# Optimization experiments

Measured on AMD Instinct MI355X. Metric: run time of the kernel, lower is better.

## Reference

```python
import jax, jax.numpy as jnp
import numpy as np

NUM_POINTS = 17
T_MAX = 2.0
VAR_GAMMA = 1.0
EPS = 1e-8


def setup_inputs() -> dict:
    key = jax.random.key(0)
    k1, k2 = jax.random.split(key)
    embeddings = jax.random.normal(k1, (65536, 768), dtype=jnp.float32)
    directions = jax.random.normal(k2, (768, 64), dtype=jnp.float32)
    return {"embeddings": embeddings, "directions": directions}


def reference(embeddings, directions):
    z = embeddings.astype(jnp.float32)  # [B, D]

    # per-dim variance floor (torch .std is unbiased, ddof=1)
    cls_std = jnp.std(z, axis=0, ddof=1)
    var_floor = jnp.mean(jax.nn.relu(VAR_GAMMA - cls_std))

    # column-normalized random directions (F.normalize(dim=0))
    dirs = directions / jnp.linalg.norm(directions, axis=0, keepdims=True)
    proj = z @ dirs  # [B, S]
    std = jnp.std(proj, axis=0, ddof=1)
    proj = (proj - jnp.mean(proj, axis=0, keepdims=True)) / (std + EPS)

    # trapezoidal quadrature over t in (0, T_MAX]
    t = jnp.linspace(0.0, T_MAX, NUM_POINTS + 1)[1:]  # [T]
    dt = T_MAX / NUM_POINTS
    w = jnp.full((NUM_POINTS,), dt).at[0].set(dt / 2).at[-1].set(dt / 2)

    # ECF over all t at once: tp [T, B, S]
    tp = t[:, None, None] * proj[None]
    ecf_real = jnp.mean(jnp.cos(tp), axis=1)  # [T, S]
    ecf_imag = jnp.mean(jnp.sin(tp), axis=1)  # [T, S]
    ecf_sq = ecf_real ** 2 + ecf_imag ** 2
    tcf = jnp.exp(-0.5 * t ** 2)[:, None]  # [T, 1]
    per_t = jnp.mean(ecf_sq - 2.0 * ecf_real * tcf + tcf ** 2, axis=1)  # [T]
    total = jnp.sum(w * per_t)

    loss = total + var_floor
    return loss
```

## Files before the change

kernel.cpp:

```cpp
#include <hip/hip_runtime.h>
#include <math.h>

#define B_ROWS 65536
#define D_DIM  768
#define S_DIM  64
#define T_PTS  17

#define WS_COLSUM 0
#define WS_COLSQ  768
#define WS_PSUM   1536
#define WS_PSQ    1600
#define WS_ECFR   1664
#define WS_ECFI   2752
#define WS_INVN   3840
#define WS_PROJ   4096

__global__ void norm_kernel(const float* __restrict__ dirs, float* __restrict__ ws) {
    int s = blockIdx.x;
    int t = threadIdx.x;
    if (s < 60) ws[s * 64 + t] = 0.f;
    float sum = 0.f;
    #pragma unroll
    for (int j = 0; j < D_DIM / 64; ++j) {
        float v = dirs[(size_t)(t + j * 64) * S_DIM + s];
        sum += v * v;
    }
    #pragma unroll
    for (int off = 32; off > 0; off >>= 1)
        sum += __shfl_down(sum, off, 64);
    if (t == 0) ws[WS_INVN + s] = 1.0f / sqrtf(sum);
}

__global__ __launch_bounds__(256) void gemm_kernel(const float* __restrict__ z,
                                                   const float* __restrict__ dirs,
                                                   float* __restrict__ ws) {
    __shared__ float smem[4352 + 4096];
    __shared__ float red_s[16 * 64];
    __shared__ float red_q[16 * 64];
    float* zsT = smem;
    float* dsm = smem + 4352;
    float* proj = ws + WS_PROJ;

    int tid = threadIdx.x;
    int tx = tid & 15, ty = tid >> 4;
    size_t rowbase = (size_t)blockIdx.x * 64;

    float4 invn4 = *reinterpret_cast<const float4*>(ws + WS_INVN + tx * 4);
    float acc[4][4] = {};

    for (int c = 0; c < D_DIM / 64; ++c) {
        int kc = c * 64;
        float ps0 = 0, ps1 = 0, ps2 = 0, ps3 = 0;
        float pq0 = 0, pq1 = 0, pq2 = 0, pq3 = 0;
        #pragma unroll
        for (int j = 0; j < 4; ++j) {
            int rr = ty + 16 * j;
            float4 v = *reinterpret_cast<const float4*>(
                z + (rowbase + rr) * D_DIM + kc + tx * 4);
            zsT[(tx * 4 + 0) * 68 + rr] = v.x;
            zsT[(tx * 4 + 1) * 68 + rr] = v.y;
            zsT[(tx * 4 + 2) * 68 + rr] = v.z;
            zsT[(tx * 4 + 3) * 68 + rr] = v.w;
            ps0 += v.x; pq0 = fmaf(v.x, v.x, pq0);
            ps1 += v.y; pq1 = fmaf(v.y, v.y, pq1);
            ps2 += v.z; pq2 = fmaf(v.z, v.z, pq2);
            ps3 += v.w; pq3 = fmaf(v.w, v.w, pq3);
            float4 dv = *reinterpret_cast<const float4*>(
                dirs + (size_t)(kc + rr) * S_DIM + tx * 4);
            dv.x *= invn4.x; dv.y *= invn4.y; dv.z *= invn4.z; dv.w *= invn4.w;
            *reinterpret_cast<float4*>(dsm + rr * 64 + tx * 4) = dv;
        }
        red_s[ty * 64 + tx * 4 + 0] = ps0;  red_q[ty * 64 + tx * 4 + 0] = pq0;
        red_s[ty * 64 + tx * 4 + 1] = ps1;  red_q[ty * 64 + tx * 4 + 1] = pq1;
        red_s[ty * 64 + tx * 4 + 2] = ps2;  red_q[ty * 64 + tx * 4 + 2] = pq2;
        red_s[ty * 64 + tx * 4 + 3] = ps3;  red_q[ty * 64 + tx * 4 + 3] = pq3;
        __syncthreads();

        if (tid < 64) {
            float ss = 0, qq = 0;
            #pragma unroll
            for (int r = 0; r < 16; ++r) {
                ss += red_s[r * 64 + tid];
                qq += red_q[r * 64 + tid];
            }
            atomicAdd(&ws[WS_COLSUM + kc + tid], ss);
            atomicAdd(&ws[WS_COLSQ + kc + tid], qq);
        }

        #pragma unroll 8
        for (int k = 0; k < 64; ++k) {
            float4 a4 = *reinterpret_cast<const float4*>(zsT + k * 68 + ty * 4);
            float4 b4 = *reinterpret_cast<const float4*>(dsm + k * 64 + tx * 4);
            float av[4] = {a4.x, a4.y, a4.z, a4.w};
            float bv[4] = {b4.x, b4.y, b4.z, b4.w};
            #pragma unroll
            for (int i = 0; i < 4; ++i)
                #pragma unroll
                for (int j = 0; j < 4; ++j)
                    acc[i][j] = fmaf(av[i], bv[j], acc[i][j]);
        }
        __syncthreads();
    }

    #pragma unroll
    for (int i = 0; i < 4; ++i) {
        float4 v = {acc[i][0], acc[i][1], acc[i][2], acc[i][3]};
        *reinterpret_cast<float4*>(proj + (rowbase + ty * 4 + i) * S_DIM + tx * 4) = v;
    }

    float cs[4] = {}, cq[4] = {};
    #pragma unroll
    for (int i = 0; i < 4; ++i)
        #pragma unroll
        for (int j = 0; j < 4; ++j) {
            cs[j] += acc[i][j];
            cq[j] = fmaf(acc[i][j], acc[i][j], cq[j]);
        }
    __syncthreads();
    #pragma unroll
    for (int j = 0; j < 4; ++j) {
        red_s[ty * 64 + tx * 4 + j] = cs[j];
        red_q[ty * 64 + tx * 4 + j] = cq[j];
    }
    __syncthreads();
    if (tid < 64) {
        float ssum = 0, qsum = 0;
        #pragma unroll
        for (int r = 0; r < 16; ++r) {
            ssum += red_s[r * 64 + tid];
            qsum += red_q[r * 64 + tid];
        }
        atomicAdd(&ws[WS_PSUM + tid], ssum);
        atomicAdd(&ws[WS_PSQ + tid],  qsum);
    }
}

__global__ __launch_bounds__(256) void ecf_kernel(float* __restrict__ ws) {
    const float* proj = ws + WS_PROJ;
    int tid = threadIdx.x;
    int s = tid & 63, r = tid >> 6;

    __shared__ float s_mean[64], s_scale[64];
    if (tid < 64) {
        float sum = ws[WS_PSUM + tid], sq = ws[WS_PSQ + tid];
        float mean = sum / (float)B_ROWS;
        float var = (sq - (float)B_ROWS * mean * mean) / (float)(B_ROWS - 1);
        var = fmaxf(var, 0.f);
        s_mean[tid]  = mean;
        s_scale[tid] = 1.0f / (sqrtf(var) + 1e-8f);
    }
    __syncthreads();
    float mean  = s_mean[s];
    float scale = s_scale[s];
    const float dt = 2.0f / 17.0f;

    float ar[T_PTS] = {}, ai[T_PTS] = {};
    size_t base = (size_t)blockIdx.x * 64;
    for (int i = 0; i < 16; ++i) {
        size_t row = base + i * 4 + r;
        float p  = proj[row * S_DIM + s];
        float ph = (p - mean) * scale;
        float a  = dt * ph;
        float s1, c1;
        __sincosf(a, &s1, &c1);
        float cc = c1, sn = s1;
        ar[0] += cc; ai[0] += sn;
        #pragma unroll
        for (int k = 1; k < T_PTS; ++k) {
            float cn = cc * c1 - sn * s1;
            sn = fmaf(sn, c1, cc * s1);
            cc = cn;
            ar[k] += cc; ai[k] += sn;
        }
    }

    __shared__ float red[3 * 2 * T_PTS * 64];
    if (r > 0) {
        float* dst = red + (r - 1) * (2 * T_PTS * 64);
        #pragma unroll
        for (int k = 0; k < T_PTS; ++k) {
            dst[k * 64 + s]               = ar[k];
            dst[T_PTS * 64 + k * 64 + s]  = ai[k];
        }
    }
    __syncthreads();
    if (r == 0) {
        const int STRIDE = 2 * T_PTS * 64;
        #pragma unroll
        for (int k = 0; k < T_PTS; ++k) {
            float vr = ar[k] + red[k * 64 + s] + red[STRIDE + k * 64 + s]
                             + red[2 * STRIDE + k * 64 + s];
            float vi = ai[k] + red[T_PTS * 64 + k * 64 + s]
                             + red[STRIDE + T_PTS * 64 + k * 64 + s]
                             + red[2 * STRIDE + T_PTS * 64 + k * 64 + s];
            atomicAdd(&ws[WS_ECFR + k * 64 + s], vr);
            atomicAdd(&ws[WS_ECFI + k * 64 + s], vi);
        }
    }
}

__global__ __launch_bounds__(256) void loss_kernel(const float* __restrict__ ws,
                                                   float* __restrict__ out) {
    int tid = threadIdx.x;
    double local = 0.0;
    for (int d = tid; d < D_DIM; d += 256) {
        double sum = (double)ws[WS_COLSUM + d];
        double sq  = (double)ws[WS_COLSQ + d];
        double mean = sum / 65536.0;
        double var  = (sq - 65536.0 * mean * mean) / 65535.0;
        if (var < 0) var = 0;
        double rl = 1.0 - sqrt(var);
        if (rl < 0) rl = 0;
        local += rl / 768.0;
    }
    const double dt = 2.0 / 17.0;
    for (int idx = tid; idx < T_PTS * 64; idx += 256) {
        int i = idx >> 6;
        double t   = dt * (i + 1);
        double tcf = exp(-0.5 * t * t);
        double w   = (i == 0 || i == T_PTS - 1) ? dt * 0.5 : dt;
        double er = (double)ws[WS_ECFR + idx] / 65536.0;
        double ei = (double)ws[WS_ECFI + idx] / 65536.0;
        double term = er * er + ei * ei - 2.0 * er * tcf + tcf * tcf;
        local += w * term / 64.0;
    }
    __shared__ double red[256];
    red[tid] = local;
    __syncthreads();
    for (int off = 128; off > 0; off >>= 1) {
        if (tid < off) red[tid] += red[tid + off];
        __syncthreads();
    }
    if (tid == 0) out[0] = (float)red[0];
}

extern "C" void kernel_launch(void* const* d_in, const int* in_sizes, int n_in,
                              void* d_out, int out_size, void* d_ws, size_t ws_size,
                              hipStream_t stream) {
    const float* z    = (const float*)d_in[0];
    const float* dirs = (const float*)d_in[1];
    float* out = (float*)d_out;
    float* ws  = (float*)d_ws;

    norm_kernel<<<S_DIM, 64, 0, stream>>>(dirs, ws);
    gemm_kernel<<<B_ROWS / 64, 256, 0, stream>>>(z, dirs, ws);
    ecf_kernel<<<B_ROWS / 64, 256, 0, stream>>>(ws);
    loss_kernel<<<1, 256, 0, stream>>>(ws, out);
}
```

Measured before the change: 397.7 us.

## Split column stats into dedicated blocks and enlarge GEMM row tile

```diff
diff --git a/kernel.cpp b/kernel.cpp
--- a/kernel.cpp
+++ b/kernel.cpp
@@ -5,6 +5,9 @@
 #define D_DIM  768
 #define S_DIM  64
 #define T_PTS  17
+
+#define GEMM_BLOCKS  512
+#define CSTAT_BLOCKS 1024
 
 #define WS_COLSUM 0
 #define WS_COLSQ  768
@@ -31,104 +34,104 @@
     if (t == 0) ws[WS_INVN + s] = 1.0f / sqrtf(sum);
 }
 
-__global__ __launch_bounds__(256) void gemm_kernel(const float* __restrict__ z,
-                                                   const float* __restrict__ dirs,
-                                                   float* __restrict__ ws) {
-    __shared__ float smem[4352 + 4096];
-    __shared__ float red_s[16 * 64];
-    __shared__ float red_q[16 * 64];
-    float* zsT = smem;
-    float* dsm = smem + 4352;
+__global__ __launch_bounds__(256, 3) void main_kernel(const float* __restrict__ z,
+                                                      const float* __restrict__ dirs,
+                                                      float* __restrict__ ws) {
+    int tid = threadIdx.x;
+
+    if (blockIdx.x >= GEMM_BLOCKS) {
+        size_t base = (size_t)(blockIdx.x - GEMM_BLOCKS) * 64 * D_DIM;
+        float s0 = 0, s1 = 0, s2 = 0, q0 = 0, q1 = 0, q2 = 0;
+        #pragma unroll 4
+        for (int r = 0; r < 64; ++r) {
+            const float* p = z + base + (size_t)r * D_DIM;
+            float a = p[tid], b = p[tid + 256], c = p[tid + 512];
+            s0 += a; q0 = fmaf(a, a, q0);
+            s1 += b; q1 = fmaf(b, b, q1);
+            s2 += c; q2 = fmaf(c, c, q2);
+        }
+        atomicAdd(&ws[WS_COLSUM + tid],       s0);
+        atomicAdd(&ws[WS_COLSUM + tid + 256], s1);
+        atomicAdd(&ws[WS_COLSUM + tid + 512], s2);
+        atomicAdd(&ws[WS_COLSQ + tid],        q0);
+        atomicAdd(&ws[WS_COLSQ + tid + 256],  q1);
+        atomicAdd(&ws[WS_COLSQ + tid + 512],  q2);
+        return;
+    }
+
+    __shared__ float zs[128 * 68];
+    __shared__ float dsm[64 * 64];
     float* proj = ws + WS_PROJ;
 
-    int tid = threadIdx.x;
     int tx = tid & 15, ty = tid >> 4;
-    size_t rowbase = (size_t)blockIdx.x * 64;
+    size_t rowbase = (size_t)blockIdx.x * 128;
 
     float4 invn4 = *reinterpret_cast<const float4*>(ws + WS_INVN + tx * 4);
-    float acc[4][4] = {};
+    float acc[8][4] = {};
 
     for (int c = 0; c < D_DIM / 64; ++c) {
         int kc = c * 64;
-        float ps0 = 0, ps1 = 0, ps2 = 0, ps3 = 0;
-        float pq0 = 0, pq1 = 0, pq2 = 0, pq3 = 0;
+        #pragma unroll
+        for (int j = 0; j < 8; ++j) {
+            int rr = ty + 16 * j;
+            *reinterpret_cast<float4*>(&zs[rr * 68 + tx * 4]) =
+                *reinterpret_cast<const float4*>(z + (rowbase + rr) * D_DIM + kc + tx * 4);
+        }
         #pragma unroll
         for (int j = 0; j < 4; ++j) {
             int rr = ty + 16 * j;
-            float4 v = *reinterpret_cast<const float4*>(
-                z + (rowbase + rr) * D_DIM + kc + tx * 4);
-            zsT[(tx * 4 + 0) * 68 + rr] = v.x;
-            zsT[(tx * 4 + 1) * 68 + rr] = v.y;
-            zsT[(tx * 4 + 2) * 68 + rr] = v.z;
-            zsT[(tx * 4 + 3) * 68 + rr] = v.w;
-            ps0 += v.x; pq0 = fmaf(v.x, v.x, pq0);
-            ps1 += v.y; pq1 = fmaf(v.y, v.y, pq1);
-            ps2 += v.z; pq2 = fmaf(v.z, v.z, pq2);
-            ps3 += v.w; pq3 = fmaf(v.w, v.w, pq3);
             float4 dv = *reinterpret_cast<const float4*>(
                 dirs + (size_t)(kc + rr) * S_DIM + tx * 4);
             dv.x *= invn4.x; dv.y *= invn4.y; dv.z *= invn4.z; dv.w *= invn4.w;
-            *reinterpret_cast<float4*>(dsm + rr * 64 + tx * 4) = dv;
-        }
-        red_s[ty * 64 + tx * 4 + 0] = ps0;  red_q[ty * 64 + tx * 4 + 0] = pq0;
-        red_s[ty * 64 + tx * 4 + 1] = ps1;  red_q[ty * 64 + tx * 4 + 1] = pq1;
-        red_s[ty * 64 + tx * 4 + 2] = ps2;  red_q[ty * 64 + tx * 4 + 2] = pq2;
-        red_s[ty * 64 + tx * 4 + 3] = ps3;  red_q[ty * 64 + tx * 4 + 3] = pq3;
+            *reinterpret_cast<float4*>(&dsm[rr * 64 + tx * 4]) = dv;
+        }
         __syncthreads();
 
-        if (tid < 64) {
-            float ss = 0, qq = 0;
+        const float* zrow = zs + ty * 8 * 68;
+        #pragma unroll 4
+        for (int k = 0; k < 64; ++k) {
+            float4 b4 = *reinterpret_cast<const float4*>(&dsm[k * 64 + tx * 4]);
             #pragma unroll
-            for (int r = 0; r < 16; ++r) {
-                ss += red_s[r * 64 + tid];
-                qq += red_q[r * 64 + tid];
+            for (int i = 0; i < 8; ++i) {
+                float a = zrow[i * 68 + k];
+                acc[i][0] = fmaf(a, b4.x, acc[i][0]);
+                acc[i][1] = fmaf(a, b4.y, acc[i][1]);
+                acc[i][2] = fmaf(a, b4.z, acc[i][2]);
+                acc[i][3] = fmaf(a, b4.w, acc[i][3]);
             }
-            atomicAdd(&ws[WS_COLSUM + kc + tid], ss);
-            atomicAdd(&ws[WS_COLSQ + kc + tid], qq);
-        }
-
-        #pragma unroll 8
-        for (int k = 0; k < 64; ++k) {
-            float4 a4 = *reinterpret_cast<const float4*>(zsT + k * 68 + ty * 4);
-            float4 b4 = *reinterpret_cast<const float4*>(dsm + k * 64 + tx * 4);
-            float av[4] = {a4.x, a4.y, a4.z, a4.w};
-            float bv[4] = {b4.x, b4.y, b4.z, b4.w};
-            #pragma unroll
-            for (int i = 0; i < 4; ++i)
-                #pragma unroll
-                for (int j = 0; j < 4; ++j)
-                    acc[i][j] = fmaf(av[i], bv[j], acc[i][j]);
         }
         __syncthreads();
     }
 
     #pragma unroll
-    for (int i = 0; i < 4; ++i) {
+    for (int i = 0; i < 8; ++i) {
         float4 v = {acc[i][0], acc[i][1], acc[i][2], acc[i][3]};
-        *reinterpret_cast<float4*>(proj + (rowbase + ty * 4 + i) * S_DIM + tx * 4) = v;
+        *reinterpret_cast<float4*>(proj + (rowbase + ty * 8 + i) * S_DIM + tx * 4) = v;
     }
 
     float cs[4] = {}, cq[4] = {};
     #pragma unroll
-    for (int i = 0; i < 4; ++i)
+    for (int i = 0; i < 8; ++i)
         #pragma unroll
         for (int j = 0; j < 4; ++j) {
             cs[j] += acc[i][j];
             cq[j] = fmaf(acc[i][j], acc[i][j], cq[j]);
         }
     __syncthreads();
+    float* reds = zs;
+    float* redq = zs + 1024;
     #pragma unroll
     for (int j = 0; j < 4; ++j) {
-        red_s[ty * 64 + tx * 4 + j] = cs[j];
-        red_q[ty * 64 + tx * 4 + j] = cq[j];
+        reds[ty * 64 + tx * 4 + j] = cs[j];
+        redq[ty * 64 + tx * 4 + j] = cq[j];
     }
     __syncthreads();
     if (tid < 64) {
         float ssum = 0, qsum = 0;
         #pragma unroll
         for (int r = 0; r < 16; ++r) {
-            ssum += red_s[r * 64 + tid];
-            qsum += red_q[r * 64 + tid];
+            ssum += reds[r * 64 + tid];
+            qsum += redq[r * 64 + tid];
         }
         atomicAdd(&ws[WS_PSUM + tid], ssum);
         atomicAdd(&ws[WS_PSQ + tid],  qsum);
@@ -243,7 +246,7 @@
     float* ws  = (float*)d_ws;
 
     norm_kernel<<<S_DIM, 64, 0, stream>>>(dirs, ws);
-    gemm_kernel<<<B_ROWS / 64, 256, 0, stream>>>(z, dirs, ws);
+    main_kernel<<<GEMM_BLOCKS + CSTAT_BLOCKS, 256, 0, stream>>>(z, dirs, ws);
     ecf_kernel<<<B_ROWS / 64, 256, 0, stream>>>(ws);
     loss_kernel<<<1, 256, 0, stream>>>(ws, out);
 }
```

Result: faster. 350.9 us (-11.8%).

## Replace FP32 FMA projection GEMM with split-bf16 three-pass MFMA

Applied to the files above, without the earlier changes.

```diff
diff --git a/kernel.cpp b/kernel.cpp
--- a/kernel.cpp
+++ b/kernel.cpp
@@ -12,126 +12,189 @@
 #define WS_PSQ    1600
 #define WS_ECFR   1664
 #define WS_ECFI   2752
-#define WS_INVN   3840
-#define WS_PROJ   4096
+#define WS_BT_HI_S 7680
+#define WS_BT_LO_S 56832
+#define WS_PROJ   53248
+
+typedef __attribute__((ext_vector_type(8))) short short8;
+typedef __attribute__((ext_vector_type(4))) short short4v;
+typedef __attribute__((ext_vector_type(4))) float float4v;
+
+#define MFMA_BF16 __builtin_amdgcn_mfma_f32_16x16x32_bf16
+
+static __device__ inline unsigned short f2bf(float x) {
+    unsigned u = __float_as_uint(x);
+    u += 0x7FFFu + ((u >> 16) & 1u);
+    return (unsigned short)(u >> 16);
+}
+static __device__ inline float bf2f(unsigned short h) {
+    return __uint_as_float(((unsigned)h) << 16);
+}
 
 __global__ void norm_kernel(const float* __restrict__ dirs, float* __restrict__ ws) {
     int s = blockIdx.x;
     int t = threadIdx.x;
     if (s < 60) ws[s * 64 + t] = 0.f;
+
     float sum = 0.f;
     #pragma unroll
-    for (int j = 0; j < D_DIM / 64; ++j) {
+    for (int j = 0; j < 12; ++j) {
         float v = dirs[(size_t)(t + j * 64) * S_DIM + s];
         sum += v * v;
     }
     #pragma unroll
-    for (int off = 32; off > 0; off >>= 1)
-        sum += __shfl_down(sum, off, 64);
-    if (t == 0) ws[WS_INVN + s] = 1.0f / sqrtf(sum);
-}
-
-__global__ __launch_bounds__(256) void gemm_kernel(const float* __restrict__ z,
-                                                   const float* __restrict__ dirs,
-                                                   float* __restrict__ ws) {
-    __shared__ float smem[4352 + 4096];
-    __shared__ float red_s[16 * 64];
-    __shared__ float red_q[16 * 64];
-    float* zsT = smem;
-    float* dsm = smem + 4352;
+    for (int m = 32; m; m >>= 1) sum += __shfl_xor(sum, m, 64);
+    float invn = 1.0f / sqrtf(sum);
+
+    unsigned short* bt_hi = (unsigned short*)ws + WS_BT_HI_S;
+    unsigned short* bt_lo = (unsigned short*)ws + WS_BT_LO_S;
+    #pragma unroll
+    for (int j = 0; j < 12; ++j) {
+        int k = t + j * 64;
+        float v = dirs[(size_t)k * S_DIM + s] * invn;
+        unsigned short hi = f2bf(v);
+        unsigned short lo = f2bf(v - bf2f(hi));
+        bt_hi[s * D_DIM + k] = hi;
+        bt_lo[s * D_DIM + k] = lo;
+    }
+}
+
+__global__ __launch_bounds__(256, 2) void main_kernel(const float* __restrict__ z,
+                                                      float* __restrict__ ws) {
+    __shared__ __align__(16) short zs_hi[128 * 72];
+    __shared__ __align__(16) short zs_lo[128 * 72];
+    __shared__ __align__(16) short bs_hi[64 * 72];
+    __shared__ __align__(16) short bs_lo[64 * 72];
+    __shared__ __align__(16) float cbuf[2 * 64 * 17];
+
+    const unsigned short* bt_hi = (const unsigned short*)ws + WS_BT_HI_S;
+    const unsigned short* bt_lo = (const unsigned short*)ws + WS_BT_LO_S;
     float* proj = ws + WS_PROJ;
 
     int tid = threadIdx.x;
     int tx = tid & 15, ty = tid >> 4;
-    size_t rowbase = (size_t)blockIdx.x * 64;
-
-    float4 invn4 = *reinterpret_cast<const float4*>(ws + WS_INVN + tx * 4);
-    float acc[4][4] = {};
+    int l = tid & 63, l15 = l & 15, q = l >> 4;
+    int waveId = tid >> 6;
+    int waveRow = waveId * 32;
+    size_t rowbase = (size_t)blockIdx.x * 128;
+
+    float4v acc[2][4] = {};
 
     for (int c = 0; c < D_DIM / 64; ++c) {
         int kc = c * 64;
+
         float ps0 = 0, ps1 = 0, ps2 = 0, ps3 = 0;
         float pq0 = 0, pq1 = 0, pq2 = 0, pq3 = 0;
         #pragma unroll
-        for (int j = 0; j < 4; ++j) {
+        for (int j = 0; j < 8; ++j) {
             int rr = ty + 16 * j;
             float4 v = *reinterpret_cast<const float4*>(
                 z + (rowbase + rr) * D_DIM + kc + tx * 4);
-            zsT[(tx * 4 + 0) * 68 + rr] = v.x;
-            zsT[(tx * 4 + 1) * 68 + rr] = v.y;
-            zsT[(tx * 4 + 2) * 68 + rr] = v.z;
-            zsT[(tx * 4 + 3) * 68 + rr] = v.w;
             ps0 += v.x; pq0 = fmaf(v.x, v.x, pq0);
             ps1 += v.y; pq1 = fmaf(v.y, v.y, pq1);
             ps2 += v.z; pq2 = fmaf(v.z, v.z, pq2);
             ps3 += v.w; pq3 = fmaf(v.w, v.w, pq3);
-            float4 dv = *reinterpret_cast<const float4*>(
-                dirs + (size_t)(kc + rr) * S_DIM + tx * 4);
-            dv.x *= invn4.x; dv.y *= invn4.y; dv.z *= invn4.z; dv.w *= invn4.w;
-            *reinterpret_cast<float4*>(dsm + rr * 64 + tx * 4) = dv;
-        }
-        red_s[ty * 64 + tx * 4 + 0] = ps0;  red_q[ty * 64 + tx * 4 + 0] = pq0;
-        red_s[ty * 64 + tx * 4 + 1] = ps1;  red_q[ty * 64 + tx * 4 + 1] = pq1;
-        red_s[ty * 64 + tx * 4 + 2] = ps2;  red_q[ty * 64 + tx * 4 + 2] = pq2;
-        red_s[ty * 64 + tx * 4 + 3] = ps3;  red_q[ty * 64 + tx * 4 + 3] = pq3;
+            short4v h4, l4;
+            h4.x = (short)f2bf(v.x); l4.x = (short)f2bf(v.x - bf2f((unsigned short)h4.x));
+            h4.y = (short)f2bf(v.y); l4.y = (short)f2bf(v.y - bf2f((unsigned short)h4.y));
+            h4.z = (short)f2bf(v.z); l4.z = (short)f2bf(v.z - bf2f((unsigned short)h4.z));
+            h4.w = (short)f2bf(v.w); l4.w = (short)f2bf(v.w - bf2f((unsigned short)h4.w));
+            *reinterpret_cast<short4v*>(&zs_hi[rr * 72 + tx * 4]) = h4;
+            *reinterpret_cast<short4v*>(&zs_lo[rr * 72 + tx * 4]) = l4;
+        }
+        cbuf[(tx * 4 + 0) * 17 + ty] = ps0;  cbuf[1088 + (tx * 4 + 0) * 17 + ty] = pq0;
+        cbuf[(tx * 4 + 1) * 17 + ty] = ps1;  cbuf[1088 + (tx * 4 + 1) * 17 + ty] = pq1;
+        cbuf[(tx * 4 + 2) * 17 + ty] = ps2;  cbuf[1088 + (tx * 4 + 2) * 17 + ty] = pq2;
+        cbuf[(tx * 4 + 3) * 17 + ty] = ps3;  cbuf[1088 + (tx * 4 + 3) * 17 + ty] = pq3;
+
+        {
+            int srow = tid >> 2;
+            int kpart = (tid & 3) * 16;
+            short8 b0 = *(const short8*)(bt_hi + (size_t)srow * D_DIM + kc + kpart);
+            short8 b1 = *(const short8*)(bt_hi + (size_t)srow * D_DIM + kc + kpart + 8);
+            short8 c0 = *(const short8*)(bt_lo + (size_t)srow * D_DIM + kc + kpart);
+            short8 c1 = *(const short8*)(bt_lo + (size_t)srow * D_DIM + kc + kpart + 8);
+            *(short8*)&bs_hi[srow * 72 + kpart]     = b0;
+            *(short8*)&bs_hi[srow * 72 + kpart + 8] = b1;
+            *(short8*)&bs_lo[srow * 72 + kpart]     = c0;
+            *(short8*)&bs_lo[srow * 72 + kpart + 8] = c1;
+        }
         __syncthreads();
 
-        if (tid < 64) {
-            float ss = 0, qq = 0;
+        if (tid < 128) {
+            int which = tid >> 6, kcol = tid & 63;
+            const float* src = cbuf + which * 1088 + kcol * 17;
+            float v = 0.f;
             #pragma unroll
-            for (int r = 0; r < 16; ++r) {
-                ss += red_s[r * 64 + tid];
-                qq += red_q[r * 64 + tid];
+            for (int r = 0; r < 16; ++r) v += src[r];
+            atomicAdd(&ws[(which ? WS_COLSQ : WS_COLSUM) + kc + kcol], v);
+        }
+
+        short8 ah[2][2], al[2][2];
+        #pragma unroll
+        for (int rt = 0; rt < 2; ++rt) {
+            int aoff = (waveRow + rt * 16 + l15) * 72 + q * 8;
+            ah[rt][0] = *(const short8*)&zs_hi[aoff];
+            ah[rt][1] = *(const short8*)&zs_hi[aoff + 32];
+            al[rt][0] = *(const short8*)&zs_lo[aoff];
+            al[rt][1] = *(const short8*)&zs_lo[aoff + 32];
+        }
+        #pragma unroll
+        for (int st = 0; st < 4; ++st) {
+            int boff = (st * 16 + l15) * 72 + q * 8;
+            short8 bh0 = *(const short8*)&bs_hi[boff];
+            short8 bh1 = *(const short8*)&bs_hi[boff + 32];
+            short8 bl0 = *(const short8*)&bs_lo[boff];
+            short8 bl1 = *(const short8*)&bs_lo[boff + 32];
+            #pragma unroll
+            for (int rt = 0; rt < 2; ++rt) {
+                acc[rt][st] = MFMA_BF16(ah[rt][0], bh0, acc[rt][st], 0, 0, 0);
+                acc[rt][st] = MFMA_BF16(al[rt][0], bh0, acc[rt][st], 0, 0, 0);
+                acc[rt][st] = MFMA_BF16(ah[rt][0], bl0, acc[rt][st], 0, 0, 0);
+                acc[rt][st] = MFMA_BF16(ah[rt][1], bh1, acc[rt][st], 0, 0, 0);
+                acc[rt][st] = MFMA_BF16(al[rt][1], bh1, acc[rt][st], 0, 0, 0);
+                acc[rt][st] = MFMA_BF16(ah[rt][1], bl1, acc[rt][st], 0, 0, 0);
             }
-            atomicAdd(&ws[WS_COLSUM + kc + tid], ss);
-            atomicAdd(&ws[WS_COLSQ + kc + tid], qq);
-        }
-
-        #pragma unroll 8
-        for (int k = 0; k < 64; ++k) {
-            float4 a4 = *reinterpret_cast<const float4*>(zsT + k * 68 + ty * 4);
-            float4 b4 = *reinterpret_cast<const float4*>(dsm + k * 64 + tx * 4);
-            float av[4] = {a4.x, a4.y, a4.z, a4.w};
-            float bv[4] = {b4.x, b4.y, b4.z, b4.w};
-            #pragma unroll
-            for (int i = 0; i < 4; ++i)
-                #pragma unroll
-                for (int j = 0; j < 4; ++j)
-                    acc[i][j] = fmaf(av[i], bv[j], acc[i][j]);
         }
         __syncthreads();
     }
 
     #pragma unroll
-    for (int i = 0; i < 4; ++i) {
-        float4 v = {acc[i][0], acc[i][1], acc[i][2], acc[i][3]};
-        *reinterpret_cast<float4*>(proj + (rowbase + ty * 4 + i) * S_DIM + tx * 4) = v;
-    }
-
-    float cs[4] = {}, cq[4] = {};
-    #pragma unroll
-    for (int i = 0; i < 4; ++i)
-        #pragma unroll
-        for (int j = 0; j < 4; ++j) {
-            cs[j] += acc[i][j];
-            cq[j] = fmaf(acc[i][j], acc[i][j], cq[j]);
-        }
+    for (int rt = 0; rt < 2; ++rt)
+        #pragma unroll
+        for (int st = 0; st < 4; ++st) {
+            int col = st * 16 + l15;
+            size_t rbase = rowbase + waveRow + rt * 16 + q * 4;
+            float4v v = acc[rt][st];
+            proj[(rbase + 0) * S_DIM + col] = v[0];
+            proj[(rbase + 1) * S_DIM + col] = v[1];
+            proj[(rbase + 2) * S_DIM + col] = v[2];
+            proj[(rbase + 3) * S_DIM + col] = v[3];
+        }
+
+    float* red = cbuf;
+    #pragma unroll
+    for (int st = 0; st < 4; ++st) {
+        float cs = 0.f, cq = 0.f;
+        #pragma unroll
+        for (int rt = 0; rt < 2; ++rt) {
+            float4v v = acc[rt][st];
+            cs += v[0] + v[1] + v[2] + v[3];
+            cq += v[0]*v[0] + v[1]*v[1] + v[2]*v[2] + v[3]*v[3];
+        }
+        int s = st * 16 + l15;
+        int slot = waveId * 4 + q;
+        red[(0 * 64 + s) * 16 + slot] = cs;
+        red[(1 * 64 + s) * 16 + slot] = cq;
+    }
     __syncthreads();
-    #pragma unroll
-    for (int j = 0; j < 4; ++j) {
-        red_s[ty * 64 + tx * 4 + j] = cs[j];
-        red_q[ty * 64 + tx * 4 + j] = cq[j];
-    }
-    __syncthreads();
-    if (tid < 64) {
-        float ssum = 0, qsum = 0;
-        #pragma unroll
-        for (int r = 0; r < 16; ++r) {
-            ssum += red_s[r * 64 + tid];
-            qsum += red_q[r * 64 + tid];
-        }
-        atomicAdd(&ws[WS_PSUM + tid], ssum);
-        atomicAdd(&ws[WS_PSQ + tid],  qsum);
+    if (tid < 128) {
+        int which = tid >> 6, s = tid & 63;
+        const float* src = red + (which * 64 + s) * 16;
+        float v = 0.f;
+        #pragma unroll
+        for (int r = 0; r < 16; ++r) v += src[r];
+        atomicAdd(&ws[(which ? WS_PSQ : WS_PSUM) + s], v);
     }
 }
 
@@ -243,7 +306,7 @@
     float* ws  = (float*)d_ws;
 
     norm_kernel<<<S_DIM, 64, 0, stream>>>(dirs, ws);
-    gemm_kernel<<<B_ROWS / 64, 256, 0, stream>>>(z, dirs, ws);
+    main_kernel<<<B_ROWS / 128, 256, 0, stream>>>(z, ws);
     ecf_kernel<<<B_ROWS / 64, 256, 0, stream>>>(ws);
     loss_kernel<<<1, 256, 0, stream>>>(ws, out);
 }
```

Measured after the change: 336.2 us. 15.5% less time.
